# Optimization experiments

Hardware: AMD Instinct MI355X
Metric: run time of the kernel (lower is better)

## Reference

```python
import jax, jax.numpy as jnp
import numpy as np

B, S, D, H, E, TOP_K = 4, 2048, 1024, 2048, 8, 2


def setup_inputs() -> dict:
    key = jax.random.key(0)
    ks = jax.random.split(key, 5)
    scale_d = 1.0 / np.sqrt(D)
    scale_h = 1.0 / np.sqrt(H)
    return {
        "x": jax.random.normal(ks[0], (B, S, D), dtype=jnp.float32),
        "gate_w": jax.random.normal(ks[1], (D, E), dtype=jnp.float32) * scale_d,
        "w1": jax.random.normal(ks[2], (E, D, H), dtype=jnp.float32) * scale_d,
        "w2": jax.random.normal(ks[3], (E, D, H), dtype=jnp.float32) * scale_d,
        "w3": jax.random.normal(ks[4], (E, H, D), dtype=jnp.float32) * scale_h,
    }


def reference(x, gate_w, w1, w2, w3):
    # Gating: softmax over experts, keep top-k probs, renormalize.
    gate_scores = jax.nn.softmax(x @ gate_w, axis=-1)          # [B,S,E]
    top_vals, top_idx = jax.lax.top_k(gate_scores, TOP_K)      # [B,S,K]
    mask = (jax.nn.one_hot(top_idx, E, dtype=x.dtype) * top_vals[..., None]).sum(axis=-2)  # [B,S,E]
    weights = mask / (mask.sum(axis=-1, keepdims=True) + 1e-9)
    # Dense SwiGLU over ALL experts (faithful to the original ModuleList loop).
    g = jax.nn.silu(jnp.einsum('bsd,edh->bseh', x, w1)) * jnp.einsum('bsd,edh->bseh', x, w2)  # [B,S,E,H]
    expert_out = jnp.einsum('bseh,ehd->bsed', g, w3)           # [B,S,E,D]
    # Masked weighted combine (dropout is identity in eval / p=0).
    return jnp.einsum('bse,bsed->bsd', weights, expert_out)    # [B,S,D]
```

## Files before the change

kernel.cpp:

```cpp
#include <hip/hip_runtime.h>

#define T_TOK 8192
#define DDIM 1024
#define HDIM 2048
#define NEXP 8

typedef __attribute__((ext_vector_type(8))) short short8;
typedef __attribute__((ext_vector_type(4))) float f32x4;

#define WAITV8 asm volatile("s_waitcnt vmcnt(8)" ::: "memory")
#define WAITV0 asm volatile("s_waitcnt vmcnt(0)" ::: "memory")
#define WAITL0 asm volatile("s_waitcnt lgkmcnt(0)" ::: "memory")
#define SCHEDB __builtin_amdgcn_sched_barrier(0)
#define BARRIER __builtin_amdgcn_s_barrier()

__device__ __forceinline__ unsigned short f2bf(float f) {
  unsigned int u = __builtin_bit_cast(unsigned int, f);
  u += 0x7fffu + ((u >> 16) & 1u);
  return (unsigned short)(u >> 16);
}
__device__ __forceinline__ float bf2f(unsigned short h) {
  unsigned int u = ((unsigned int)h) << 16;
  return __builtin_bit_cast(float, u);
}
__device__ __forceinline__ void gload16(const void* g, void* l) {
  __builtin_amdgcn_global_load_lds((const __attribute__((address_space(1))) void*)g,
                                   (__attribute__((address_space(3))) void*)l, 16, 0, 0);
}
__device__ __forceinline__ int imin(int a, int b) { return a < b ? a : b; }

__global__ __launch_bounds__(256) void cvt_kernel(const float* __restrict__ in,
                                                  unsigned short* __restrict__ out, int n) {
  int i = (blockIdx.x * 256 + threadIdx.x) * 8;
  int stride = gridDim.x * 256 * 8;
  for (; i < n; i += stride) {
    float4 a = *(const float4*)(in + i);
    float4 b = *(const float4*)(in + i + 4);
    alignas(16) unsigned short t[8] = {f2bf(a.x), f2bf(a.y), f2bf(a.z), f2bf(a.w),
                                       f2bf(b.x), f2bf(b.y), f2bf(b.z), f2bf(b.w)};
    *(uint4*)(out + i) = *(const uint4*)t;
  }
}

__global__ __launch_bounds__(256) void tcvt_kernel(const float* __restrict__ in,
                                                   unsigned short* __restrict__ out,
                                                   int R, int C, size_t outEstride,
                                                   int perm, int s16) {
  int e = blockIdx.z;
  int rb = blockIdx.y * 64, cb = blockIdx.x * 64;
  const float* inE = in + (size_t)e * R * C;
  unsigned short* outE = out + (size_t)e * outEstride;
  __shared__ float tile[64][65];
  int tid = threadIdx.x;
  #pragma unroll
  for (int i = 0; i < 4; ++i) {
    int f = tid + i * 256;
    int r = f >> 4, c4 = (f & 15) << 2;
    float4 v = *(const float4*)(inE + (size_t)(rb + r) * C + cb + c4);
    tile[r][c4] = v.x; tile[r][c4 + 1] = v.y; tile[r][c4 + 2] = v.z; tile[r][c4 + 3] = v.w;
  }
  __syncthreads();
  #pragma unroll
  for (int i = 0; i < 2; ++i) {
    int g = tid + i * 256;
    int oc = g >> 3;
    int r8 = (g & 7) << 3;
    alignas(16) unsigned short tmp[8];
    #pragma unroll
    for (int j = 0; j < 8; ++j) tmp[j] = f2bf(tile[r8 + j][oc]);
    int orow = cb + oc;
    int orow2 = perm ? (32 * (orow >> 4) + (orow & 15) + s16) : orow;
    *(uint4*)(outE + (size_t)orow2 * R + rb + r8) = *(const uint4*)tmp;
  }
}

__global__ __launch_bounds__(256) void gate_kernel(const float* __restrict__ x,
                                                   const float* __restrict__ gw,
                                                   int* __restrict__ t_exp,
                                                   float* __restrict__ t_w) {
  int t = blockIdx.x * 4 + (threadIdx.x >> 6);
  int lane = threadIdx.x & 63;
  const float* xp = x + (size_t)t * DDIM;
  float acc[NEXP];
  #pragma unroll
  for (int e = 0; e < NEXP; ++e) acc[e] = 0.f;
  for (int i = 0; i < DDIM / 64; ++i) {
    int d = i * 64 + lane;
    float xv = xp[d];
    const float* g = gw + d * NEXP;
    #pragma unroll
    for (int e = 0; e < NEXP; ++e) acc[e] += xv * g[e];
  }
  #pragma unroll
  for (int off = 32; off > 0; off >>= 1) {
    #pragma unroll
    for (int e = 0; e < NEXP; ++e) acc[e] += __shfl_xor(acc[e], off, 64);
  }
  float mx = acc[0];
  #pragma unroll
  for (int e = 1; e < NEXP; ++e) mx = fmaxf(mx, acc[e]);
  float p[NEXP]; float S = 0.f;
  #pragma unroll
  for (int e = 0; e < NEXP; ++e) { p[e] = expf(acc[e] - mx); S += p[e]; }
  int i0 = 0; float v0 = p[0];
  #pragma unroll
  for (int e = 1; e < NEXP; ++e) if (p[e] > v0) { v0 = p[e]; i0 = e; }
  int i1 = -1; float v1 = -1.f;
  #pragma unroll
  for (int e = 0; e < NEXP; ++e) if (e != i0 && p[e] > v1) { v1 = p[e]; i1 = e; }
  float pv0 = v0 / S, pv1 = v1 / S;
  float denom = pv0 + pv1 + 1e-9f;
  if (lane == 0) {
    t_exp[t * 2] = i0; t_exp[t * 2 + 1] = i1;
    t_w[t * 2] = pv0 / denom; t_w[t * 2 + 1] = pv1 / denom;
  }
}

__global__ __launch_bounds__(1024) void partition_kernel(
    const int* __restrict__ t_exp, const float* __restrict__ t_w,
    int* __restrict__ ctrl, int* __restrict__ row_tok,
    float* __restrict__ row_w, int* __restrict__ inv_row) {
  int tid = threadIdx.x;
  int wv = tid >> 6, lane = tid & 63;
  __shared__ int wtot[16][8];
  __shared__ int wbase[16][8];
  __shared__ int soff[8];

  int t0 = tid * 8;
  int exps[16];
  int c[8];
  #pragma unroll
  for (int e = 0; e < 8; ++e) c[e] = 0;
  #pragma unroll
  for (int s = 0; s < 16; ++s) {
    exps[s] = t_exp[t0 * 2 + s];
    #pragma unroll
    for (int e = 0; e < 8; ++e) c[e] += (exps[s] == e);
  }
  int inc[8];
  #pragma unroll
  for (int e = 0; e < 8; ++e) inc[e] = c[e];
  #pragma unroll
  for (int d = 1; d < 64; d <<= 1) {
    #pragma unroll
    for (int e = 0; e < 8; ++e) {
      int v = __shfl_up(inc[e], d, 64);
      if (lane >= d) inc[e] += v;
    }
  }
  if (lane == 63) {
    #pragma unroll
    for (int e = 0; e < 8; ++e) wtot[wv][e] = inc[e];
  }
  __syncthreads();
  if (wv == 0 && lane < 16) {
    #pragma unroll
    for (int e = 0; e < 8; ++e) {
      int b = 0;
      for (int w = 0; w < 16; ++w)
        if (w < lane) b += wtot[w][e];
      wbase[lane][e] = b;
    }
  }
  __syncthreads();
  if (tid == 0) {
    int o = 0;
    #pragma unroll
    for (int e = 0; e < 8; ++e) {
      int tot = wbase[15][e] + wtot[15][e];
      ctrl[e] = tot; ctrl[8 + e] = o; soff[e] = o; o += tot;
    }
  }
  __syncthreads();
  int base[8];
  #pragma unroll
  for (int e = 0; e < 8; ++e) base[e] = soff[e] + wbase[wv][e] + (inc[e] - c[e]);
  #pragma unroll
  for (int s = 0; s < 16; ++s) {
    int ee = exps[s];
    float w = t_w[t0 * 2 + s];
    int pos = 0;
    #pragma unroll
    for (int e = 0; e < 8; ++e)
      if (ee == e) { pos = base[e]; base[e] = base[e] + 1; }
    row_tok[pos] = t0 + (s >> 1);
    row_w[pos] = w;
    inv_row[t0 * 2 + s] = pos;
  }
}


__global__ __launch_bounds__(512, 2) void gemm1_kernel(
    const unsigned short* __restrict__ xbf,
    const unsigned short* __restrict__ w12t,
    const int* __restrict__ row_tok, const float* __restrict__ row_w,
    const int* __restrict__ ctrl, unsigned short* __restrict__ G) {
  int bid = blockIdx.x;
  int e = bid & 7;
  int j = bid >> 3;
  int nt = ((j >> 6) << 2) | (j & 3);
  int mt0 = (j >> 2) & 15;
  int cnt = ctrl[e];
  if (mt0 * 256 >= cnt) return;
  int off = ctrl[8 + e];

  __shared__ unsigned short lds[2][2][256 * 64];

  int tid = threadIdx.x, lane = tid & 63;
  const unsigned short* w12e = w12t + (size_t)e * (4096 * 1024);

  int rr = tid >> 3, cc = tid & 7;
  int clog8 = (cc ^ (rr & 7)) * 8;
  const unsigned short* bp[4];
  #pragma unroll
  for (int r = 0; r < 4; ++r)
    bp[r] = w12e + (size_t)(nt * 256 + r * 64 + rr) * 1024 + clog8;

  int wid = tid >> 6, wr = wid >> 2, wc = wid & 3;
  int lr16 = lane & 15, hi = lane >> 4, rk = lr16 & 7;
  int k0o = (hi ^ rk) * 8;
  int k1o = ((4 | hi) ^ rk) * 8;
  int abase = (wr * 128 + lr16) * 64;
  int bbase = (wc * 64 + lr16) * 64;

#define STG1(B, KT) do { int _k = (KT) * 64;                              \
    gload16(ap[0] + _k, &lds[B][0][0] + (0 * 512 + tid) * 8);             \
    gload16(ap[1] + _k, &lds[B][0][0] + (1 * 512 + tid) * 8);             \
    gload16(ap[2] + _k, &lds[B][0][0] + (2 * 512 + tid) * 8);             \
    gload16(ap[3] + _k, &lds[B][0][0] + (3 * 512 + tid) * 8);             \
    gload16(bp[0] + _k, &lds[B][1][0] + (0 * 512 + tid) * 8);             \
    gload16(bp[1] + _k, &lds[B][1][0] + (1 * 512 + tid) * 8);             \
    gload16(bp[2] + _k, &lds[B][1][0] + (2 * 512 + tid) * 8);             \
    gload16(bp[3] + _k, &lds[B][1][0] + (3 * 512 + tid) * 8); } while (0)

#define READF(B, KO, AV, BV) do {                                         \
    const unsigned short* _A = &lds[B][0][0];                             \
    const unsigned short* _Bp = &lds[B][1][0];                            \
    _Pragma("unroll")                                                     \
    for (int m = 0; m < 8; ++m) AV[m] = *(const short8*)(_A + abase + m * 1024 + KO); \
    _Pragma("unroll")                                                     \
    for (int n = 0; n < 4; ++n) BV[n] = *(const short8*)(_Bp + bbase + n * 1024 + KO); } while (0)

#define MF(AV, BV) do {                                                   \
    __builtin_amdgcn_s_setprio(1);                                        \
    _Pragma("unroll")                                                     \
    for (int m = 0; m < 8; ++m)                                           \
      _Pragma("unroll")                                                   \
      for (int n = 0; n < 4; ++n)                                         \
        acc[m][n] = __builtin_amdgcn_mfma_f32_16x16x32_bf16(AV[m], BV[n], acc[m][n], 0, 0, 0); \
    __builtin_amdgcn_s_setprio(0); } while (0)

  #pragma unroll 1
  for (int mt = mt0; mt * 256 < cnt; mt += 16) {
    const unsigned short* ap[4];
    #pragma unroll
    for (int r = 0; r < 4; ++r) {
      int tok = row_tok[off + imin(mt * 256 + r * 64 + rr, cnt - 1)];
      ap[r] = xbf + (size_t)tok * 1024 + clog8;
    }
    f32x4 z = {0.f, 0.f, 0.f, 0.f};
    f32x4 acc[8][4];
    #pragma unroll
    for (int m = 0; m < 8; ++m)
      #pragma unroll
      for (int n = 0; n < 4; ++n) acc[m][n] = z;

    STG1(0, 0);
    STG1(1, 1);
    #pragma unroll 1
    for (int kt = 0; kt < 16; ++kt) {
      int cb = kt & 1;
      if (kt + 1 < 16) { WAITV8; } else { WAITV0; }
      SCHEDB;
      BARRIER;
      short8 av[8], bv[4], av2[8], bv2[4];
      READF(cb, k0o, av, bv);
      READF(cb, k1o, av2, bv2);
      MF(av, bv);
      WAITL0; SCHEDB;
      BARRIER;
      if (kt + 2 < 16) STG1(cb, kt + 2);
      SCHEDB;
      MF(av2, bv2);
    }

    #pragma unroll
    for (int m = 0; m < 8; ++m)
      #pragma unroll
      for (int jj = 0; jj < 4; ++jj) {
        int rl = mt * 256 + wr * 128 + m * 16 + hi * 4 + jj;
        if (rl < cnt) {
          float wrj = row_w[off + rl];
          size_t base = (size_t)(off + rl) * HDIM + nt * 128 + wc * 32 + lr16;
          float h1 = acc[m][0][jj], h2 = acc[m][1][jj];
          G[base] = f2bf((h1 / (1.f + __expf(-h1))) * h2 * wrj);
          h1 = acc[m][2][jj]; h2 = acc[m][3][jj];
          G[base + 16] = f2bf((h1 / (1.f + __expf(-h1))) * h2 * wrj);
        }
      }
  }
#undef STG1
}

__global__ __launch_bounds__(512, 2) void gemm2_kernel(
    const unsigned short* __restrict__ G,
    const unsigned short* __restrict__ w3t,
    const int* __restrict__ ctrl, unsigned short* __restrict__ Y) {
  int bid = blockIdx.x;
  int e = bid & 7;
  int j = bid >> 3;
  int nt = j & 3;
  int mt0 = j >> 2;
  int cnt = ctrl[e];
  if (mt0 * 256 >= cnt) return;
  int off = ctrl[8 + e];

  __shared__ unsigned short lds[2][2][256 * 64];

  int tid = threadIdx.x, lane = tid & 63;
  const unsigned short* w3e = w3t + (size_t)e * (1024 * 2048);

  int rr = tid >> 3, cc = tid & 7;
  int clog8 = (cc ^ (rr & 7)) * 8;
  const unsigned short* bp[4];
  #pragma unroll
  for (int r = 0; r < 4; ++r)
    bp[r] = w3e + (size_t)(nt * 256 + r * 64 + rr) * 2048 + clog8;

  int wid = tid >> 6, wr = wid >> 2, wc = wid & 3;
  int lr16 = lane & 15, hi = lane >> 4, rk = lr16 & 7;
  int k0o = (hi ^ rk) * 8;
  int k1o = ((4 | hi) ^ rk) * 8;
  int abase = (wr * 128 + lr16) * 64;
  int bbase = (wc * 64 + lr16) * 64;

#define STG2(B, KT) do { int _k = (KT) * 64;                              \
    gload16(ap[0] + _k, &lds[B][0][0] + (0 * 512 + tid) * 8);             \
    gload16(ap[1] + _k, &lds[B][0][0] + (1 * 512 + tid) * 8);             \
    gload16(ap[2] + _k, &lds[B][0][0] + (2 * 512 + tid) * 8);             \
    gload16(ap[3] + _k, &lds[B][0][0] + (3 * 512 + tid) * 8);             \
    gload16(bp[0] + _k, &lds[B][1][0] + (0 * 512 + tid) * 8);             \
    gload16(bp[1] + _k, &lds[B][1][0] + (1 * 512 + tid) * 8);             \
    gload16(bp[2] + _k, &lds[B][1][0] + (2 * 512 + tid) * 8);             \
    gload16(bp[3] + _k, &lds[B][1][0] + (3 * 512 + tid) * 8); } while (0)

  #pragma unroll 1
  for (int mt = mt0; mt * 256 < cnt; mt += 16) {
    const unsigned short* ap[4];
    #pragma unroll
    for (int r = 0; r < 4; ++r)
      ap[r] = G + (size_t)(off + imin(mt * 256 + r * 64 + rr, cnt - 1)) * 2048 + clog8;

    f32x4 z = {0.f, 0.f, 0.f, 0.f};
    f32x4 acc[8][4];
    #pragma unroll
    for (int m = 0; m < 8; ++m)
      #pragma unroll
      for (int n = 0; n < 4; ++n) acc[m][n] = z;

    STG2(0, 0);
    STG2(1, 1);
    #pragma unroll 1
    for (int kt = 0; kt < 32; ++kt) {
      int cb = kt & 1;
      if (kt + 1 < 32) { WAITV8; } else { WAITV0; }
      SCHEDB;
      BARRIER;
      short8 av[8], bv[4], av2[8], bv2[4];
      READF(cb, k0o, av, bv);
      READF(cb, k1o, av2, bv2);
      MF(av, bv);
      WAITL0; SCHEDB;
      BARRIER;
      if (kt + 2 < 32) STG2(cb, kt + 2);
      SCHEDB;
      MF(av2, bv2);
    }

    #pragma unroll
    for (int m = 0; m < 8; ++m)
      #pragma unroll
      for (int jj = 0; jj < 4; ++jj) {
        int rl = mt * 256 + wr * 128 + m * 16 + hi * 4 + jj;
        if (rl < cnt) {
          size_t yrow = (size_t)(off + rl) * DDIM + nt * 256 + wc * 64 + lr16;
          #pragma unroll
          for (int n = 0; n < 4; ++n) Y[yrow + n * 16] = f2bf(acc[m][n][jj]);
        }
      }
  }
#undef STG2
#undef READF
#undef MF
}

__global__ __launch_bounds__(256) void combine_kernel(const unsigned short* __restrict__ Y,
                                                      const int* __restrict__ inv_row,
                                                      float* __restrict__ out) {
  int gid = blockIdx.x * 256 + threadIdx.x;
  int t = gid >> 7;
  int cidx = (gid & 127) * 8;
  int rA = inv_row[t * 2], rB = inv_row[t * 2 + 1];
  uint4 va = *(const uint4*)(Y + (size_t)rA * DDIM + cidx);
  uint4 vb = *(const uint4*)(Y + (size_t)rB * DDIM + cidx);
  const unsigned short* pa = (const unsigned short*)&va;
  const unsigned short* pb = (const unsigned short*)&vb;
  float4 o0, o1;
  o0.x = bf2f(pa[0]) + bf2f(pb[0]); o0.y = bf2f(pa[1]) + bf2f(pb[1]);
  o0.z = bf2f(pa[2]) + bf2f(pb[2]); o0.w = bf2f(pa[3]) + bf2f(pb[3]);
  o1.x = bf2f(pa[4]) + bf2f(pb[4]); o1.y = bf2f(pa[5]) + bf2f(pb[5]);
  o1.z = bf2f(pa[6]) + bf2f(pb[6]); o1.w = bf2f(pa[7]) + bf2f(pb[7]);
  float* op = out + (size_t)t * DDIM + cidx;
  *(float4*)op = o0;
  *(float4*)(op + 4) = o1;
}

extern "C" void kernel_launch(void* const* d_in, const int* in_sizes, int n_in,
                              void* d_out, int out_size, void* d_ws, size_t ws_size,
                              hipStream_t stream) {
  const float* x  = (const float*)d_in[0];
  const float* gw = (const float*)d_in[1];
  const float* w1 = (const float*)d_in[2];
  const float* w2 = (const float*)d_in[3];
  const float* w3 = (const float*)d_in[4];
  float* out = (float*)d_out;
  char* ws = (char*)d_ws;

  unsigned short* xbf  = (unsigned short*)(ws + 0);
  unsigned short* w12t = (unsigned short*)(ws + 16777216);
  unsigned short* w3t  = (unsigned short*)(ws + 83886080);
  unsigned short* G    = (unsigned short*)(ws + 117440512);
  unsigned short* Y    = (unsigned short*)(ws + 184549376);
  int*   row_tok = (int*)  (ws + 218103808);
  float* row_w   = (float*)(ws + 218169344);
  int*   inv_row = (int*)  (ws + 218234880);
  int*   t_exp   = (int*)  (ws + 218300416);
  float* t_w     = (float*)(ws + 218365952);
  int*   ctrl    = (int*)  (ws + 218431488);

  cvt_kernel<<<4096, 256, 0, stream>>>(x, xbf, T_TOK * DDIM);
  tcvt_kernel<<<dim3(32, 16, 8), 256, 0, stream>>>(w1, w12t, 1024, 2048,
                                                   (size_t)4096 * 1024, 1, 0);
  tcvt_kernel<<<dim3(32, 16, 8), 256, 0, stream>>>(w2, w12t, 1024, 2048,
                                                   (size_t)4096 * 1024, 1, 16);
  tcvt_kernel<<<dim3(16, 32, 8), 256, 0, stream>>>(w3, w3t, 2048, 1024,
                                                   (size_t)1024 * 2048, 0, 0);

  gate_kernel<<<2048, 256, 0, stream>>>(x, gw, t_exp, t_w);
  partition_kernel<<<1, 1024, 0, stream>>>(t_exp, t_w, ctrl, row_tok, row_w, inv_row);

  gemm1_kernel<<<2048, 512, 0, stream>>>(xbf, w12t, row_tok, row_w, ctrl, G);
  gemm2_kernel<<<512, 512, 0, stream>>>(G, w3t, ctrl, Y);
  combine_kernel<<<4096, 256, 0, stream>>>(Y, inv_row, out);
}
```

Before: 413.0 us.

## Restructure MoE GEMM K-loop into eight-phase half-K pipeline with finer staging

Replaces the double-buffered 64-wide K loop in both expert GEMMs with an eight-phase schedule. Each 64-wide K tile is split into two 32-wide halves, and each half's global-to-LDS loads are interleaved with MFMA phases on half the M rows. A new XOR swizzle matches the 32-element row layout, and launch bounds drop to one block per SM. The goal is to overlap loads with MFMA at finer granularity and cut register pressure from holding both K halves of fragments. The cost is more barriers per tile and lower occupancy.

```diff
diff --git a/kernel.cpp b/kernel.cpp
--- a/kernel.cpp
+++ b/kernel.cpp
@@ -190,7 +190,58 @@
 }
 
 
-__global__ __launch_bounds__(512, 2) void gemm1_kernel(
+#define PHASE(B, KS, MH, STG, DOVM) do {                                   \
+    short8 av[4];                                                          \
+    if (MH == 0) {                                                         \
+      _Pragma("unroll")                                                    \
+      for (int n = 0; n < 4; ++n)                                          \
+        bv[n] = *(const short8*)(&lds[B][1][KS][0] + boff + n * 512);      \
+    }                                                                      \
+    _Pragma("unroll")                                                      \
+    for (int m = 0; m < 4; ++m)                                            \
+      av[m] = *(const short8*)(&lds[B][0][KS][0] + aoff + (MH * 4 + m) * 512); \
+    STG;                                                                   \
+    if (DOVM) { WAITV8; }                                                  \
+    BARRIER;                                                               \
+    WAITL0; SCHEDB;                                                        \
+    __builtin_amdgcn_s_setprio(1);                                         \
+    _Pragma("unroll")                                                      \
+    for (int m = 0; m < 4; ++m)                                            \
+      _Pragma("unroll")                                                    \
+      for (int n = 0; n < 4; ++n)                                          \
+        acc[MH * 4 + m][n] = __builtin_amdgcn_mfma_f32_16x16x32_bf16(av[m], bv[n], acc[MH * 4 + m][n], 0, 0, 0); \
+    __builtin_amdgcn_s_setprio(0);                                         \
+    BARRIER;                                                               \
+} while (0)
+
+#define STAGE_A(B, KH, KT) do { int _o = (KT) * 64 + (KH) * 32;            \
+    gload16(aSrc0 + _o, &lds[B][0][KH][0] + tid * 8);                      \
+    gload16(aSrc1 + _o, &lds[B][0][KH][0] + (512 + tid) * 8); } while (0)
+#define STAGE_B(B, KH, KT) do { int _o = (KT) * 64 + (KH) * 32;            \
+    gload16(bSrc0 + _o, &lds[B][1][KH][0] + tid * 8);                      \
+    gload16(bSrc1 + _o, &lds[B][1][KH][0] + (512 + tid) * 8); } while (0)
+
+#define K_PIPELINE(NT)                                                     \
+  WAITV0;                                                                  \
+  STAGE_A(0, 0, 0); STAGE_B(0, 0, 0);                                      \
+  STAGE_A(0, 1, 0); STAGE_B(0, 1, 0);                                      \
+  STAGE_A(1, 0, 1); STAGE_B(1, 0, 1);                                      \
+  WAITV8; BARRIER;                                                         \
+  _Pragma("unroll 1")                                                      \
+  for (int kt = 0; kt < (NT); kt += 2) {                                   \
+    int t1 = kt + 1;                                                       \
+    int t2 = imin(kt + 2, (NT) - 1), t3 = imin(kt + 3, (NT) - 1);          \
+    PHASE(0, 0, 0, STAGE_A(1, 1, t1), 0);                                  \
+    PHASE(0, 0, 1, STAGE_B(1, 1, t1), 1);                                  \
+    PHASE(0, 1, 0, STAGE_A(0, 0, t2), 0);                                  \
+    PHASE(0, 1, 1, STAGE_B(0, 0, t2), 1);                                  \
+    PHASE(1, 0, 0, STAGE_A(0, 1, t2), 0);                                  \
+    PHASE(1, 0, 1, STAGE_B(0, 1, t2), 1);                                  \
+    PHASE(1, 1, 0, STAGE_A(1, 0, t3), 0);                                  \
+    PHASE(1, 1, 1, STAGE_B(1, 0, t3), 1);                                  \
+  }
+
+__global__ __launch_bounds__(512, 1) void gemm1_kernel(
     const unsigned short* __restrict__ xbf,
     const unsigned short* __restrict__ w12t,
     const int* __restrict__ row_tok, const float* __restrict__ row_w,
@@ -204,85 +255,40 @@
   if (mt0 * 256 >= cnt) return;
   int off = ctrl[8 + e];
 
-  __shared__ unsigned short lds[2][2][256 * 64];
+  __shared__ unsigned short lds[2][2][2][8192];
 
   int tid = threadIdx.x, lane = tid & 63;
   const unsigned short* w12e = w12t + (size_t)e * (4096 * 1024);
 
-  int rr = tid >> 3, cc = tid & 7;
-  int clog8 = (cc ^ (rr & 7)) * 8;
-  const unsigned short* bp[4];
-  #pragma unroll
-  for (int r = 0; r < 4; ++r)
-    bp[r] = w12e + (size_t)(nt * 256 + r * 64 + rr) * 1024 + clog8;
+  int r0 = tid >> 2, c0 = tid & 3;
+  int r1 = 128 + r0;
+  int cs0 = (c0 ^ ((r0 >> 1) & 3)) * 8;
+  int cs1 = (c0 ^ ((r1 >> 1) & 3)) * 8;
+  const unsigned short* bSrc0 = w12e + (size_t)(nt * 256 + r0) * 1024 + cs0;
+  const unsigned short* bSrc1 = w12e + (size_t)(nt * 256 + r1) * 1024 + cs1;
 
   int wid = tid >> 6, wr = wid >> 2, wc = wid & 3;
-  int lr16 = lane & 15, hi = lane >> 4, rk = lr16 & 7;
-  int k0o = (hi ^ rk) * 8;
-  int k1o = ((4 | hi) ^ rk) * 8;
-  int abase = (wr * 128 + lr16) * 64;
-  int bbase = (wc * 64 + lr16) * 64;
-
-#define STG1(B, KT) do { int _k = (KT) * 64;                              \
-    gload16(ap[0] + _k, &lds[B][0][0] + (0 * 512 + tid) * 8);             \
-    gload16(ap[1] + _k, &lds[B][0][0] + (1 * 512 + tid) * 8);             \
-    gload16(ap[2] + _k, &lds[B][0][0] + (2 * 512 + tid) * 8);             \
-    gload16(ap[3] + _k, &lds[B][0][0] + (3 * 512 + tid) * 8);             \
-    gload16(bp[0] + _k, &lds[B][1][0] + (0 * 512 + tid) * 8);             \
-    gload16(bp[1] + _k, &lds[B][1][0] + (1 * 512 + tid) * 8);             \
-    gload16(bp[2] + _k, &lds[B][1][0] + (2 * 512 + tid) * 8);             \
-    gload16(bp[3] + _k, &lds[B][1][0] + (3 * 512 + tid) * 8); } while (0)
-
-#define READF(B, KO, AV, BV) do {                                         \
-    const unsigned short* _A = &lds[B][0][0];                             \
-    const unsigned short* _Bp = &lds[B][1][0];                            \
-    _Pragma("unroll")                                                     \
-    for (int m = 0; m < 8; ++m) AV[m] = *(const short8*)(_A + abase + m * 1024 + KO); \
-    _Pragma("unroll")                                                     \
-    for (int n = 0; n < 4; ++n) BV[n] = *(const short8*)(_Bp + bbase + n * 1024 + KO); } while (0)
-
-#define MF(AV, BV) do {                                                   \
-    __builtin_amdgcn_s_setprio(1);                                        \
-    _Pragma("unroll")                                                     \
-    for (int m = 0; m < 8; ++m)                                           \
-      _Pragma("unroll")                                                   \
-      for (int n = 0; n < 4; ++n)                                         \
-        acc[m][n] = __builtin_amdgcn_mfma_f32_16x16x32_bf16(AV[m], BV[n], acc[m][n], 0, 0, 0); \
-    __builtin_amdgcn_s_setprio(0); } while (0)
+  int lr16 = lane & 15, hi = lane >> 4;
+  int skey = (lr16 >> 1) & 3;
+  int aoff = (wr * 128 + lr16) * 32 + ((hi ^ skey) * 8);
+  int boff = (wc * 64 + lr16) * 32 + ((hi ^ skey) * 8);
 
   #pragma unroll 1
   for (int mt = mt0; mt * 256 < cnt; mt += 16) {
-    const unsigned short* ap[4];
-    #pragma unroll
-    for (int r = 0; r < 4; ++r) {
-      int tok = row_tok[off + imin(mt * 256 + r * 64 + rr, cnt - 1)];
-      ap[r] = xbf + (size_t)tok * 1024 + clog8;
-    }
+    int tokA = row_tok[off + imin(mt * 256 + r0, cnt - 1)];
+    int tokB = row_tok[off + imin(mt * 256 + r1, cnt - 1)];
+    const unsigned short* aSrc0 = xbf + (size_t)tokA * 1024 + cs0;
+    const unsigned short* aSrc1 = xbf + (size_t)tokB * 1024 + cs1;
+
     f32x4 z = {0.f, 0.f, 0.f, 0.f};
     f32x4 acc[8][4];
     #pragma unroll
     for (int m = 0; m < 8; ++m)
       #pragma unroll
       for (int n = 0; n < 4; ++n) acc[m][n] = z;
-
-    STG1(0, 0);
-    STG1(1, 1);
-    #pragma unroll 1
-    for (int kt = 0; kt < 16; ++kt) {
-      int cb = kt & 1;
-      if (kt + 1 < 16) { WAITV8; } else { WAITV0; }
-      SCHEDB;
-      BARRIER;
-      short8 av[8], bv[4], av2[8], bv2[4];
-      READF(cb, k0o, av, bv);
-      READF(cb, k1o, av2, bv2);
-      MF(av, bv);
-      WAITL0; SCHEDB;
-      BARRIER;
-      if (kt + 2 < 16) STG1(cb, kt + 2);
-      SCHEDB;
-      MF(av2, bv2);
-    }
+    short8 bv[4];
+
+    K_PIPELINE(16)
 
     #pragma unroll
     for (int m = 0; m < 8; ++m)
@@ -299,10 +305,9 @@
         }
       }
   }
-#undef STG1
-}
-
-__global__ __launch_bounds__(512, 2) void gemm2_kernel(
+}
+
+__global__ __launch_bounds__(512, 1) void gemm2_kernel(
     const unsigned short* __restrict__ G,
     const unsigned short* __restrict__ w3t,
     const int* __restrict__ ctrl, unsigned short* __restrict__ Y) {
@@ -315,41 +320,30 @@
   if (mt0 * 256 >= cnt) return;
   int off = ctrl[8 + e];
 
-  __shared__ unsigned short lds[2][2][256 * 64];
+  __shared__ unsigned short lds[2][2][2][8192];
 
   int tid = threadIdx.x, lane = tid & 63;
   const unsigned short* w3e = w3t + (size_t)e * (1024 * 2048);
 
-  int rr = tid >> 3, cc = tid & 7;
-  int clog8 = (cc ^ (rr & 7)) * 8;
-  const unsigned short* bp[4];
-  #pragma unroll
-  for (int r = 0; r < 4; ++r)
-    bp[r] = w3e + (size_t)(nt * 256 + r * 64 + rr) * 2048 + clog8;
+  int r0 = tid >> 2, c0 = tid & 3;
+  int r1 = 128 + r0;
+  int cs0 = (c0 ^ ((r0 >> 1) & 3)) * 8;
+  int cs1 = (c0 ^ ((r1 >> 1) & 3)) * 8;
+  const unsigned short* bSrc0 = w3e + (size_t)(nt * 256 + r0) * 2048 + cs0;
+  const unsigned short* bSrc1 = w3e + (size_t)(nt * 256 + r1) * 2048 + cs1;
 
   int wid = tid >> 6, wr = wid >> 2, wc = wid & 3;
-  int lr16 = lane & 15, hi = lane >> 4, rk = lr16 & 7;
-  int k0o = (hi ^ rk) * 8;
-  int k1o = ((4 | hi) ^ rk) * 8;
-  int abase = (wr * 128 + lr16) * 64;
-  int bbase = (wc * 64 + lr16) * 64;
-
-#define STG2(B, KT) do { int _k = (KT) * 64;                              \
-    gload16(ap[0] + _k, &lds[B][0][0] + (0 * 512 + tid) * 8);             \
-    gload16(ap[1] + _k, &lds[B][0][0] + (1 * 512 + tid) * 8);             \
-    gload16(ap[2] + _k, &lds[B][0][0] + (2 * 512 + tid) * 8);             \
-    gload16(ap[3] + _k, &lds[B][0][0] + (3 * 512 + tid) * 8);             \
-    gload16(bp[0] + _k, &lds[B][1][0] + (0 * 512 + tid) * 8);             \
-    gload16(bp[1] + _k, &lds[B][1][0] + (1 * 512 + tid) * 8);             \
-    gload16(bp[2] + _k, &lds[B][1][0] + (2 * 512 + tid) * 8);             \
-    gload16(bp[3] + _k, &lds[B][1][0] + (3 * 512 + tid) * 8); } while (0)
+  int lr16 = lane & 15, hi = lane >> 4;
+  int skey = (lr16 >> 1) & 3;
+  int aoff = (wr * 128 + lr16) * 32 + ((hi ^ skey) * 8);
+  int boff = (wc * 64 + lr16) * 32 + ((hi ^ skey) * 8);
 
   #pragma unroll 1
   for (int mt = mt0; mt * 256 < cnt; mt += 16) {
-    const unsigned short* ap[4];
-    #pragma unroll
-    for (int r = 0; r < 4; ++r)
-      ap[r] = G + (size_t)(off + imin(mt * 256 + r * 64 + rr, cnt - 1)) * 2048 + clog8;
+    const unsigned short* aSrc0 =
+        G + (size_t)(off + imin(mt * 256 + r0, cnt - 1)) * 2048 + cs0;
+    const unsigned short* aSrc1 =
+        G + (size_t)(off + imin(mt * 256 + r1, cnt - 1)) * 2048 + cs1;
 
     f32x4 z = {0.f, 0.f, 0.f, 0.f};
     f32x4 acc[8][4];
@@ -357,25 +351,9 @@
     for (int m = 0; m < 8; ++m)
       #pragma unroll
       for (int n = 0; n < 4; ++n) acc[m][n] = z;
-
-    STG2(0, 0);
-    STG2(1, 1);
-    #pragma unroll 1
-    for (int kt = 0; kt < 32; ++kt) {
-      int cb = kt & 1;
-      if (kt + 1 < 32) { WAITV8; } else { WAITV0; }
-      SCHEDB;
-      BARRIER;
-      short8 av[8], bv[4], av2[8], bv2[4];
-      READF(cb, k0o, av, bv);
-      READF(cb, k1o, av2, bv2);
-      MF(av, bv);
-      WAITL0; SCHEDB;
-      BARRIER;
-      if (kt + 2 < 32) STG2(cb, kt + 2);
-      SCHEDB;
-      MF(av2, bv2);
-    }
+    short8 bv[4];
+
+    K_PIPELINE(32)
 
     #pragma unroll
     for (int m = 0; m < 8; ++m)
@@ -389,9 +367,6 @@
         }
       }
   }
-#undef STG2
-#undef READF
-#undef MF
 }
 
 __global__ __launch_bounds__(256) void combine_kernel(const unsigned short* __restrict__ Y,
```

After: 393.7 us. 1.05x faster.
